# Kernel optimization log

Measured on AMD Instinct MI355X. Metric: run time of the kernel, lower is better.

## Reference

```python
import jax, jax.numpy as jnp
import numpy as np

B, S, D, H = 2, 2048, 1024, 16
EPS = 1e-7  # keras backend epsilon

def setup_inputs() -> dict:
    key = jax.random.key(0)
    ks = jax.random.split(key, 5)
    x = jax.random.normal(ks[0], (B, S, D), dtype=jnp.float32)
    # mem_mask convention: attend where mem_mask == 0 (causal here)
    i = jnp.arange(S)
    causal = (i[None, :] > i[:, None]).astype(jnp.float32)  # 1 = masked
    mem_mask = jnp.broadcast_to(causal[None, None], (B, 1, S, S))
    Wqkv = jax.random.normal(ks[1], (D, 3 * D), dtype=jnp.float32) * (D ** -0.5)
    W_out = jax.random.normal(ks[2], (D, D), dtype=jnp.float32) * (D ** -0.5)
    b_out = jnp.zeros((D,), dtype=jnp.float32)
    scale = jnp.ones((D,), dtype=jnp.float32)
    gate = jax.random.normal(ks[3], (D,), dtype=jnp.float32) * 0.02
    return {"x": x, "mem_mask": mem_mask, "Wqkv": Wqkv, "W_out": W_out,
            "b_out": b_out, "scale": scale, "gate": gate}

def reference(x, mem_mask, Wqkv, W_out, b_out, scale, gate):
    b, s, d = x.shape
    dh = d // H
    h = jnp.einsum('bsd,de->bse', x, Wqkv)
    q, k, v = jnp.split(h, 3, axis=-1)
    def split_heads(t):
        return t.reshape(b, s, H, dh).transpose(0, 2, 1, 3)  # [B,H,S,dh]
    q, k, v = split_heads(q), split_heads(k), split_heads(v)
    q = q * (dh ** -0.5)
    logits = jnp.einsum('bhqd,bhkd->bhqk', q, k)
    logits = logits * (mem_mask == 0.0).astype(logits.dtype)
    weights = jax.nn.relu(logits)
    o = jnp.einsum('bhqk,bhkd->bhqd', weights, v)
    o = o.transpose(0, 2, 1, 3).reshape(b, s, d)  # combine heads
    # Gated RMSNorm
    ms = jnp.mean(o * o, axis=-1, keepdims=True)
    o = scale * o * jax.lax.rsqrt(ms + EPS) * jax.nn.sigmoid(gate * o)
    return jnp.einsum('bsd,de->bse', o, W_out) + b_out
```

## Files before the change

kernel.cpp:

```cpp
#include <hip/hip_runtime.h>
#include <hip/hip_bf16.h>

typedef unsigned short u16;
typedef __attribute__((ext_vector_type(8))) short bf16x8;
typedef __attribute__((ext_vector_type(4))) short short4v;
typedef __attribute__((ext_vector_type(4))) float floatx4;
typedef __attribute__((ext_vector_type(2))) unsigned uint2v;

__device__ __forceinline__ float bf2f(u16 u) {
    unsigned v = ((unsigned)u) << 16;
    return __builtin_bit_cast(float, v);
}
__device__ __forceinline__ u16 f2bf(float f) {
    unsigned u = __builtin_bit_cast(unsigned, f);
    u += 0x7fffu + ((u >> 16) & 1u);
    return (u16)(u >> 16);
}

#define GLDS16(g, l)                                                             \
    __builtin_amdgcn_global_load_lds(                                            \
        (const __attribute__((address_space(1))) void*)(g),                      \
        (__attribute__((address_space(3))) void*)(l), 16, 0, 0)

__global__ __launch_bounds__(256) void cvt_bf16(const float* __restrict__ in, u16* __restrict__ out,
                                                float* __restrict__ oz) {
    const int i = blockIdx.x * 256 + threadIdx.x;
    const floatx4 v = ((const floatx4*)in)[i];
    short4v o;
#pragma unroll
    for (int j = 0; j < 4; ++j) o[j] = (short)f2bf(v[j]);
    ((short4v*)out)[i] = o;
    const floatx4 z = {0.f, 0.f, 0.f, 0.f};
    ((floatx4*)oz)[i] = z;
}

__global__ void wtrans(const float* __restrict__ in, u16* __restrict__ out, int R, int C) {
    __shared__ u16 t[32][33];
    const int c0 = blockIdx.x * 32, r0 = blockIdx.y * 32;
    const int x = threadIdx.x, y = threadIdx.y;
#pragma unroll
    for (int i = 0; i < 32; i += 8) t[y + i][x] = f2bf(in[(size_t)(r0 + y + i) * C + c0 + x]);
    __syncthreads();
#pragma unroll
    for (int i = 0; i < 32; i += 8) out[(size_t)(c0 + y + i) * R + r0 + x] = t[x][y + i];
}

__global__ void vtrans(const u16* __restrict__ h, u16* __restrict__ vt) {
    __shared__ u16 t[32][33];
    const int bh = blockIdx.z;
    const int b = bh >> 4, hd = bh & 15;
    const int s0 = blockIdx.x * 32, d0 = blockIdx.y * 32;
    const int x = threadIdx.x, y = threadIdx.y;
    const u16* in = h + (size_t)(b * 2048) * 3072 + 2048 + hd * 64;
#pragma unroll
    for (int i = 0; i < 32; i += 8) t[y + i][x] = in[(size_t)(s0 + y + i) * 3072 + d0 + x];
    __syncthreads();
    u16* o = vt + (size_t)bh * 64 * 2048;
#pragma unroll
    for (int i = 0; i < 32; i += 8) {
        const float f = bf2f(t[x][y + i]) * 0.125f;
        o[(size_t)(d0 + y + i) * 2048 + s0 + x] = (u16)(__builtin_bit_cast(unsigned, f) >> 16);
    }
}

template <int TM, bool BIAS, typename OUT>
__global__ __launch_bounds__(256) void gemm_bt(const u16* __restrict__ A, const u16* __restrict__ Bt,
                                               OUT* __restrict__ C, const float* __restrict__ bias,
                                               int M, int N, int K) {
    constexpr int MI = TM / 32;
    __shared__ u16 sA[TM * 32];
    __shared__ u16 sB[128 * 32];
    const int tid = threadIdx.x;
    const int lane = tid & 63, wave = tid >> 6;
    const int l15 = lane & 15, quad = lane >> 4;
    const int row0 = blockIdx.y * TM, col0 = blockIdx.x * 128;
    const int wm = (wave & 1) * (TM / 2), wn = (wave >> 1) * 64;
    const int c_ = (tid & 3) << 3;
    floatx4 acc[MI][4] = {};
    for (int k0 = 0; k0 < K; k0 += 32) {
#pragma unroll
        for (int it = 0; it < 2; ++it) {
            const int idx = it * 256 + tid;
            const int r = idx >> 2;
            GLDS16(Bt + (size_t)(col0 + r) * K + k0 + c_, sB + idx * 8);
        }
#pragma unroll
        for (int it = 0; it < TM / 64; ++it) {
            const int idx = it * 256 + tid;
            const int r = idx >> 2;
            GLDS16(A + (size_t)(row0 + r) * K + k0 + c_, sA + idx * 8);
        }
        __syncthreads();
        bf16x8 af[MI], bfr[4];
#pragma unroll
        for (int i = 0; i < MI; ++i) af[i] = *(const bf16x8*)(sA + (wm + i * 16 + l15) * 32 + quad * 8);
#pragma unroll
        for (int j = 0; j < 4; ++j) bfr[j] = *(const bf16x8*)(sB + (wn + j * 16 + l15) * 32 + quad * 8);
#pragma unroll
        for (int i = 0; i < MI; ++i)
#pragma unroll
            for (int j = 0; j < 4; ++j)
                acc[i][j] = __builtin_amdgcn_mfma_f32_16x16x32_bf16(af[i], bfr[j], acc[i][j], 0, 0, 0);
        __syncthreads();
    }
#pragma unroll
    for (int i = 0; i < MI; ++i) {
#pragma unroll
        for (int j = 0; j < 4; ++j) {
            const int col = col0 + wn + j * 16 + l15;
            const int row = row0 + wm + i * 16 + quad * 4;
            const float b = BIAS ? bias[col] : 0.f;
#pragma unroll
            for (int r = 0; r < 4; ++r) {
                const float v = acc[i][j][r] + b;
                if constexpr (sizeof(OUT) == 2)
                    C[(size_t)(row + r) * N + col] = (OUT)f2bf(v);
                else
                    C[(size_t)(row + r) * N + col] = (OUT)v;
            }
        }
    }
}

__device__ __forceinline__ void pack_store(floatx4 s, u16* dst, bool diag, int kgb, int qg) {
    float v0 = fmaxf(s[0], 0.f), v1 = fmaxf(s[1], 0.f);
    float v2 = fmaxf(s[2], 0.f), v3 = fmaxf(s[3], 0.f);
    if (diag) {
        if (kgb + 0 > qg) v0 = 0.f;
        if (kgb + 1 > qg) v1 = 0.f;
        if (kgb + 2 > qg) v2 = 0.f;
        if (kgb + 3 > qg) v3 = 0.f;
    }
    uint2v p;
    p.x = ((__builtin_bit_cast(unsigned, v0) + 0x8000u) >> 16) |
          ((__builtin_bit_cast(unsigned, v1) + 0x8000u) & 0xffff0000u);
    p.y = ((__builtin_bit_cast(unsigned, v2) + 0x8000u) >> 16) |
          ((__builtin_bit_cast(unsigned, v3) + 0x8000u) & 0xffff0000u);
    *(uint2v*)dst = p;
}

__global__ __launch_bounds__(256) void relu_attn(const u16* __restrict__ h, const u16* __restrict__ vt,
                                                 float* __restrict__ o) {
    __shared__ u16 sK[64 * 72];
    __shared__ u16 sV[64 * 72];
    __shared__ u16 sP[64 * 72];
    const int bid = blockIdx.x;
    const int bh = bid & 31;
    const int p = bid >> 5;
    int s, qt;
    if (p < 32)      { s = 0; qt = 31 - p; }
    else if (p < 56) { s = 1; qt = 31 - (p - 32); }
    else if (p < 72) { s = 2; qt = 31 - (p - 56); }
    else             { s = 3; qt = 31 - (p - 72); }
    const int b = bh >> 4, hd = bh & 15;
    const int tid = threadIdx.x, lane = tid & 63, wave = tid >> 6;
    const int l15 = lane & 15, quad = lane >> 4;
    const int q0 = qt * 64;
    const int c_lo = s * 8, c_hi = min(s * 8 + 7, qt);

    const u16* qrow = h + (size_t)(b * 2048 + q0 + wave * 16 + l15) * 3072 + hd * 64;
    bf16x8 qf0 = *(const bf16x8*)(qrow + quad * 8);
    bf16x8 qf1 = *(const bf16x8*)(qrow + 32 + quad * 8);

    floatx4 acc[4] = {};
    const u16* kbase = h + (size_t)(b * 2048) * 3072 + 1024 + hd * 64;
    const u16* vbase = vt + (size_t)bh * 64 * 2048;
    const int sr = tid >> 3;
    const int sc = (tid & 7) << 3;
    const int qg = wave * 16 + l15;

    for (int kc = c_lo; kc <= c_hi; ++kc) {
        const int c0 = kc * 64;
#pragma unroll
        for (int it = 0; it < 2; ++it) {
            const int r = it * 32 + sr;
            bf16x8 kv = *(const bf16x8*)(kbase + (size_t)(c0 + r) * 3072 + sc);
            bf16x8 vv = *(const bf16x8*)(vbase + (size_t)r * 2048 + c0 + sc);
            *(bf16x8*)(sK + r * 72 + sc) = kv;
            *(bf16x8*)(sV + r * 72 + sc) = vv;
        }
        __syncthreads();
        const bool diag = (kc == qt);
        const floatx4 z = {0.f, 0.f, 0.f, 0.f};
#pragma unroll
        for (int mt = 0; mt < 4; ++mt) {
            const bf16x8 kf0 = *(const bf16x8*)(sK + (mt * 16 + l15) * 72 + quad * 8);
            const bf16x8 kf1 = *(const bf16x8*)(sK + (mt * 16 + l15) * 72 + 32 + quad * 8);
            const int kgb = mt * 16 + quad * 4;
            floatx4 sv_ = __builtin_amdgcn_mfma_f32_16x16x32_bf16(kf0, qf0, z, 0, 0, 0);
            sv_ = __builtin_amdgcn_mfma_f32_16x16x32_bf16(kf1, qf1, sv_, 0, 0, 0);
            pack_store(sv_, sP + (size_t)qg * 72 + kgb, diag, kgb, qg);
        }
#pragma unroll
        for (int kb = 0; kb < 2; ++kb) {
            const bf16x8 pf = *(const bf16x8*)(sP + (size_t)(wave * 16 + l15) * 72 + kb * 32 + quad * 8);
#pragma unroll
            for (int nt = 0; nt < 4; ++nt) {
                const bf16x8 vf = *(const bf16x8*)(sV + (nt * 16 + l15) * 72 + kb * 32 + quad * 8);
                acc[nt] = __builtin_amdgcn_mfma_f32_16x16x32_bf16(pf, vf, acc[nt], 0, 0, 0);
            }
        }
        __syncthreads();
    }
#pragma unroll
    for (int nt = 0; nt < 4; ++nt) {
        const int col = hd * 64 + nt * 16 + l15;
        const int row = q0 + wave * 16 + quad * 4;
#pragma unroll
        for (int r = 0; r < 4; ++r)
            atomicAdd(&o[(size_t)(b * 2048 + row + r) * 1024 + col], acc[nt][r]);
    }
}

__global__ __launch_bounds__(256) void rms_gate(const float* __restrict__ o, const float* __restrict__ scale,
                                                const float* __restrict__ gate, u16* __restrict__ out) {
    const int row = blockIdx.x;
    const int tid = threadIdx.x;
    const floatx4* op = (const floatx4*)(o + (size_t)row * 1024);
    floatx4 v = op[tid];
    float ss = v[0] * v[0] + v[1] * v[1] + v[2] * v[2] + v[3] * v[3];
#pragma unroll
    for (int m = 32; m >= 1; m >>= 1) ss += __shfl_xor(ss, m, 64);
    __shared__ float red[4];
    if ((tid & 63) == 0) red[tid >> 6] = ss;
    __syncthreads();
    const float ms = (red[0] + red[1] + red[2] + red[3]) * (1.0f / 1024.0f);
    const float inv = rsqrtf(ms + 1e-7f);
    const int c = tid * 4;
#pragma unroll
    for (int j = 0; j < 4; ++j) {
        const float s = scale[c + j];
        const float g = gate[c + j];
        const float x = v[j];
        const float sig = 1.0f / (1.0f + __expf(-g * x));
        out[(size_t)row * 1024 + c + j] = f2bf(s * x * inv * sig);
    }
}

extern "C" void kernel_launch(void* const* d_in, const int* in_sizes, int n_in,
                              void* d_out, int out_size, void* d_ws, size_t ws_size,
                              hipStream_t stream) {
    const float* x     = (const float*)d_in[0];
    const float* Wqkv  = (const float*)d_in[2];
    const float* Wout  = (const float*)d_in[3];
    const float* bout  = (const float*)d_in[4];
    const float* scale = (const float*)d_in[5];
    const float* gate  = (const float*)d_in[6];
    float* out = (float*)d_out;

    char* p = (char*)d_ws;
    u16* xb    = (u16*)p; p += (size_t)4096 * 1024 * 2;
    u16* h     = (u16*)p; p += (size_t)4096 * 3072 * 2;
    u16* vt    = (u16*)p; p += (size_t)32 * 64 * 2048 * 2;
    u16* WqkvT = (u16*)p; p += (size_t)3072 * 1024 * 2;
    u16* WoutT = (u16*)p; p += (size_t)1024 * 1024 * 2;
    float* oat = (float*)p; p += (size_t)4096 * 1024 * 4;
    u16* onorm = (u16*)p; p += (size_t)4096 * 1024 * 2;

    cvt_bf16<<<4096, 256, 0, stream>>>(x, xb, oat);
    wtrans<<<dim3(96, 32), dim3(32, 8), 0, stream>>>(Wqkv, WqkvT, 1024, 3072);
    wtrans<<<dim3(32, 32), dim3(32, 8), 0, stream>>>(Wout, WoutT, 1024, 1024);
    gemm_bt<128, false, u16><<<dim3(24, 32), 256, 0, stream>>>(xb, WqkvT, h, nullptr, 4096, 3072, 1024);
    vtrans<<<dim3(64, 2, 32), dim3(32, 8), 0, stream>>>(h, vt);
    relu_attn<<<2560, 256, 0, stream>>>(h, vt, oat);
    rms_gate<<<4096, 256, 0, stream>>>(oat, scale, gate, onorm);
    gemm_bt<64, true, float><<<dim3(8, 64), 256, 0, stream>>>(onorm, WoutT, out, bout, 4096, 1024, 1024);
}
```

Before: 230.0 us.

## Merge prep kernels and fuse V transpose into QKV GEMM epilogue

Combines the x-to-bf16 conversion, output zeroing and both weight transposes into one prep launch. The separate vtrans kernel is removed: the QKV GEMM epilogue now also writes the pre-scaled, transposed V tile directly into vt. This cuts kernel launches and the extra read of V from h. The cost is extra strided 8-byte stores in the GEMM epilogue, and the scaling now rounds bf16 differently (round-to-nearest of v*0.125 instead of truncating the scaled bf16 value).

```diff
diff --git a/kernel.cpp b/kernel.cpp
--- a/kernel.cpp
+++ b/kernel.cpp
@@ -22,51 +22,39 @@
         (const __attribute__((address_space(1))) void*)(g),                      \
         (__attribute__((address_space(3))) void*)(l), 16, 0, 0)
 
-__global__ __launch_bounds__(256) void cvt_bf16(const float* __restrict__ in, u16* __restrict__ out,
-                                                float* __restrict__ oz) {
-    const int i = blockIdx.x * 256 + threadIdx.x;
-    const floatx4 v = ((const floatx4*)in)[i];
-    short4v o;
-#pragma unroll
-    for (int j = 0; j < 4; ++j) o[j] = (short)f2bf(v[j]);
-    ((short4v*)out)[i] = o;
-    const floatx4 z = {0.f, 0.f, 0.f, 0.f};
-    ((floatx4*)oz)[i] = z;
-}
-
-__global__ void wtrans(const float* __restrict__ in, u16* __restrict__ out, int R, int C) {
+__global__ __launch_bounds__(256) void prep(const float* __restrict__ x, u16* __restrict__ xb,
+                                            float* __restrict__ oz,
+                                            const float* __restrict__ Wqkv, u16* __restrict__ WqkvT,
+                                            const float* __restrict__ Wout, u16* __restrict__ WoutT) {
     __shared__ u16 t[32][33];
-    const int c0 = blockIdx.x * 32, r0 = blockIdx.y * 32;
-    const int x = threadIdx.x, y = threadIdx.y;
-#pragma unroll
-    for (int i = 0; i < 32; i += 8) t[y + i][x] = f2bf(in[(size_t)(r0 + y + i) * C + c0 + x]);
+    int blk = blockIdx.x;
+    if (blk < 4096) {
+        const int i = blk * 256 + threadIdx.x;
+        const floatx4 v = ((const floatx4*)x)[i];
+        short4v o;
+#pragma unroll
+        for (int j = 0; j < 4; ++j) o[j] = (short)f2bf(v[j]);
+        ((short4v*)xb)[i] = o;
+        const floatx4 z = {0.f, 0.f, 0.f, 0.f};
+        ((floatx4*)oz)[i] = z;
+        return;
+    }
+    const float* in; u16* out; int R, C, bx, by;
+    if (blk < 4096 + 3072) { blk -= 4096; in = Wqkv; out = WqkvT; R = 1024; C = 3072; bx = blk % 96; by = blk / 96; }
+    else                   { blk -= 7168; in = Wout; out = WoutT; R = 1024; C = 1024; bx = blk & 31; by = blk >> 5; }
+    const int c0 = bx * 32, r0 = by * 32;
+    const int xx = threadIdx.x & 31, yy = threadIdx.x >> 5;
+#pragma unroll
+    for (int i = 0; i < 32; i += 8) t[yy + i][xx] = f2bf(in[(size_t)(r0 + yy + i) * C + c0 + xx]);
     __syncthreads();
 #pragma unroll
-    for (int i = 0; i < 32; i += 8) out[(size_t)(c0 + y + i) * R + r0 + x] = t[x][y + i];
-}
-
-__global__ void vtrans(const u16* __restrict__ h, u16* __restrict__ vt) {
-    __shared__ u16 t[32][33];
-    const int bh = blockIdx.z;
-    const int b = bh >> 4, hd = bh & 15;
-    const int s0 = blockIdx.x * 32, d0 = blockIdx.y * 32;
-    const int x = threadIdx.x, y = threadIdx.y;
-    const u16* in = h + (size_t)(b * 2048) * 3072 + 2048 + hd * 64;
-#pragma unroll
-    for (int i = 0; i < 32; i += 8) t[y + i][x] = in[(size_t)(s0 + y + i) * 3072 + d0 + x];
-    __syncthreads();
-    u16* o = vt + (size_t)bh * 64 * 2048;
-#pragma unroll
-    for (int i = 0; i < 32; i += 8) {
-        const float f = bf2f(t[x][y + i]) * 0.125f;
-        o[(size_t)(d0 + y + i) * 2048 + s0 + x] = (u16)(__builtin_bit_cast(unsigned, f) >> 16);
-    }
-}
-
-template <int TM, bool BIAS, typename OUT>
+    for (int i = 0; i < 32; i += 8) out[(size_t)(c0 + yy + i) * R + r0 + xx] = t[xx][yy + i];
+}
+
+template <int TM, bool BIAS, typename OUT, bool VT>
 __global__ __launch_bounds__(256) void gemm_bt(const u16* __restrict__ A, const u16* __restrict__ Bt,
                                                OUT* __restrict__ C, const float* __restrict__ bias,
-                                               int M, int N, int K) {
+                                               u16* __restrict__ vtp, int M, int N, int K) {
     constexpr int MI = TM / 32;
     __shared__ u16 sA[TM * 32];
     __shared__ u16 sB[128 * 32];
@@ -110,6 +98,7 @@
             const int col = col0 + wn + j * 16 + l15;
             const int row = row0 + wm + i * 16 + quad * 4;
             const float b = BIAS ? bias[col] : 0.f;
+            short4v pk;
 #pragma unroll
             for (int r = 0; r < 4; ++r) {
                 const float v = acc[i][j][r] + b;
@@ -117,6 +106,14 @@
                     C[(size_t)(row + r) * N + col] = (OUT)f2bf(v);
                 else
                     C[(size_t)(row + r) * N + col] = (OUT)v;
+                if constexpr (VT) pk[r] = (short)f2bf(v * 0.125f);
+            }
+            if constexpr (VT) {
+                if (col0 >= 2048) {
+                    const int bb = row >> 11, s = row & 2047;
+                    const int hd = (col - 2048) >> 6, dh = col & 63;
+                    *(short4v*)(vtp + ((size_t)(bb * 16 + hd) * 64 + dh) * 2048 + s) = pk;
+                }
             }
         }
     }
@@ -257,12 +254,9 @@
     float* oat = (float*)p; p += (size_t)4096 * 1024 * 4;
     u16* onorm = (u16*)p; p += (size_t)4096 * 1024 * 2;
 
-    cvt_bf16<<<4096, 256, 0, stream>>>(x, xb, oat);
-    wtrans<<<dim3(96, 32), dim3(32, 8), 0, stream>>>(Wqkv, WqkvT, 1024, 3072);
-    wtrans<<<dim3(32, 32), dim3(32, 8), 0, stream>>>(Wout, WoutT, 1024, 1024);
-    gemm_bt<128, false, u16><<<dim3(24, 32), 256, 0, stream>>>(xb, WqkvT, h, nullptr, 4096, 3072, 1024);
-    vtrans<<<dim3(64, 2, 32), dim3(32, 8), 0, stream>>>(h, vt);
+    prep<<<8192, 256, 0, stream>>>(x, xb, oat, Wqkv, WqkvT, Wout, WoutT);
+    gemm_bt<128, false, u16, true><<<dim3(24, 32), 256, 0, stream>>>(xb, WqkvT, h, nullptr, vt, 4096, 3072, 1024);
     relu_attn<<<2560, 256, 0, stream>>>(h, vt, oat);
     rms_gate<<<4096, 256, 0, stream>>>(oat, scale, gate, onorm);
-    gemm_bt<64, true, float><<<dim3(8, 64), 256, 0, stream>>>(onorm, WoutT, out, bout, 4096, 1024, 1024);
-}
+    gemm_bt<64, true, float, false><<<dim3(8, 64), 256, 0, stream>>>(onorm, WoutT, out, bout, nullptr, 4096, 1024, 1024);
+}
```

Result: faster. 223.6 us (-2.8%).
